# Kernel tuning notes

Measured on AMD Instinct MI355X. Metric: run time of the kernel, lower is better.

Reference implementation:

```python
import jax, jax.numpy as jnp
import numpy as np
import math

B, S, D, H = 8, 1024, 1024, 16
DK = D          # d_k = d_v = d_model (required for the per-head matmul to type-check)
HD = DK // H    # per-head dim = 64


def setup_inputs() -> dict:
    key = jax.random.key(0)
    ks = jax.random.split(key, 10)
    sc = 0.02
    return {
        "source": jax.random.normal(ks[0], (B, S, D), dtype=jnp.float32),
        "target": jax.random.normal(ks[1], (B, S, D), dtype=jnp.float32),
        "wq": jax.random.normal(ks[2], (D, DK), dtype=jnp.float32) * sc,
        "wk": jax.random.normal(ks[3], (D, DK), dtype=jnp.float32) * sc,
        "wv": jax.random.normal(ks[4], (D, DK), dtype=jnp.float32) * sc,
        "WQ": jax.random.normal(ks[5], (H, D, HD), dtype=jnp.float32) * sc,
        "WK": jax.random.normal(ks[6], (H, D, HD), dtype=jnp.float32) * sc,
        "WV": jax.random.normal(ks[7], (H, D, HD), dtype=jnp.float32) * sc,
        "ow": jax.random.normal(ks[8], (DK, D), dtype=jnp.float32) * sc,
        "ob": jnp.zeros((D,), dtype=jnp.float32),
    }


def reference(source, target, wq, wk, wv, WQ, WK, WV, ow, ob):
    # shared projections (nn.Linear, bias=False)
    Q = source @ wq          # (B,S,DK)
    K = target @ wk          # (B,S,DK)
    V = target @ wv          # (B,S,DK)
    # per-head projections Q @ W_Q[i], vectorized over all heads
    q = jnp.einsum('bsk,hkd->bhsd', Q, WQ)   # (B,H,S,HD)
    k = jnp.einsum('bsk,hkd->bhsd', K, WK)
    v = jnp.einsum('bsk,hkd->bhsd', V, WV)
    scores = jnp.einsum('bhqd,bhkd->bhqk', q, k) / math.sqrt(DK)
    # NOTE: original uses nn.Softmax(dim=1) on (B, Sq, Sk) -> normalizes over
    # the QUERY axis; faithful translation => axis=2 of (B,H,Sq,Sk).
    attn = jax.nn.softmax(scores, axis=2)
    o = jnp.einsum('bhqk,bhkd->bhqd', attn, v)          # (B,H,S,HD)
    o = jnp.transpose(o, (0, 2, 1, 3)).reshape(B, S, DK)  # concat heads
    return o @ ow + ob
```

## Files before the change

kernel.cpp:

```cpp
#include <hip/hip_runtime.h>

using u16 = unsigned short;
typedef float f32x4 __attribute__((ext_vector_type(4)));
typedef __bf16 bf16x8 __attribute__((ext_vector_type(8)));
typedef unsigned short u16x4 __attribute__((ext_vector_type(4)));
typedef unsigned short u16x8 __attribute__((ext_vector_type(8)));
typedef unsigned int u32x2 __attribute__((ext_vector_type(2)));

static constexpr float SC2 = 0.03125f * 1.44269504088896f;

static __device__ __forceinline__ u16 f2bf(float f) {
  unsigned u = __builtin_bit_cast(unsigned, f);
  u += 0x7FFFu + ((u >> 16) & 1u);
  return (u16)(u >> 16);
}
static __device__ __forceinline__ float bf2f(u16 h) {
  unsigned u = ((unsigned)h) << 16;
  return __builtin_bit_cast(float, u);
}
static __device__ __forceinline__ unsigned cvt_pk(float lo, float hi) {
  unsigned r;
  asm("v_cvt_pk_bf16_f32 %0, %1, %2" : "=v"(r) : "v"(lo), "v"(hi));
  return r;
}

typedef __attribute__((address_space(3))) unsigned int lds_uint;
typedef __attribute__((address_space(1))) unsigned int g_uint;

static __device__ __forceinline__ void load_lds16(const u16* gp, const void* lp) {
  __builtin_amdgcn_global_load_lds((g_uint*)(unsigned long long)gp,
                                   (lds_uint*)(unsigned int)(unsigned long long)lp,
                                   16, 0, 0);
}

struct Cast2 { const float* in[2]; u16* out[2]; };
__global__ __launch_bounds__(256) void k_cast2(Cast2 P, int n4) {
  int i = blockIdx.x * 256 + threadIdx.x;
  if (i >= n4) return;
  f32x4 v = reinterpret_cast<const f32x4*>(P.in[blockIdx.z])[i];
  u16x4 o;
  o[0] = f2bf(v[0]); o[1] = f2bf(v[1]); o[2] = f2bf(v[2]); o[3] = f2bf(v[3]);
  reinterpret_cast<u16x4*>(P.out[blockIdx.z])[i] = o;
}
struct Cast3 { const float* in[3]; u16* out[3]; };
__global__ __launch_bounds__(256) void k_cast3(Cast3 P, int n4) {
  int i = blockIdx.x * 256 + threadIdx.x;
  if (i >= n4) return;
  f32x4 v = reinterpret_cast<const f32x4*>(P.in[blockIdx.z])[i];
  u16x4 o;
  o[0] = f2bf(v[0]); o[1] = f2bf(v[1]); o[2] = f2bf(v[2]); o[3] = f2bf(v[3]);
  reinterpret_cast<u16x4*>(P.out[blockIdx.z])[i] = o;
}

__global__ __launch_bounds__(256) void k_relayout_W3(Cast3 P) {
  int idx = blockIdx.x * 256 + threadIdx.x;
  int n = idx >> 10, c = idx & 1023;
  int h = n >> 6, j = n & 63;
  P.out[blockIdx.z][idx] = f2bf(P.in[blockIdx.z][(h * 1024 + c) * 64 + j]);
}

__global__ __launch_bounds__(256) void k_relayout_owT(const float* __restrict__ ow,
                                                      u16* __restrict__ out) {
  int idx = blockIdx.x * 256 + threadIdx.x;
  int n = idx >> 10, k = idx & 1023;
  out[idx] = f2bf(ow[k * 1024 + n]);
}

struct GemmPtrs { const u16* A; const u16* B; void* C; float scale; };
struct Gemm3 { GemmPtrs g[3]; };

__global__ __launch_bounds__(256) void k_gemm_bt(Gemm3 P, int N, int K,
                                                 const float* __restrict__ bias,
                                                 int outf32) {
  const u16* A  = P.g[blockIdx.z].A;
  const u16* Bt = P.g[blockIdx.z].B;
  const float sc = P.g[blockIdx.z].scale;
  __shared__ u16 As[2][128 * 64];
  __shared__ u16 Bs[2][128 * 64];
  const int tid = threadIdx.x, lane = tid & 63, w = tid >> 6;
  const int swz = (blockIdx.x & 7) * (gridDim.x >> 3) + (blockIdx.x >> 3);
  const int nbn = N >> 7;
  const int m0 = (swz / nbn) << 7;
  const int n0 = (swz % nbn) << 7;
  const int wr = (w >> 1) << 6, wc = (w & 1) << 6;
  const int l15 = lane & 15, lg = lane >> 4;
  const int srow = tid >> 3;
  const int sslot = (tid & 7) ^ (srow & 7);
  const u16* Ag = A  + (size_t)(m0 + srow) * K + sslot * 8;
  const u16* Bg = Bt + (size_t)(n0 + srow) * K + sslot * 8;

  f32x4 acc[4][4];
#pragma unroll
  for (int i = 0; i < 4; ++i)
#pragma unroll
    for (int j = 0; j < 4; ++j) acc[i][j] = f32x4{0.f, 0.f, 0.f, 0.f};

#pragma unroll
  for (int j = 0; j < 4; ++j) {
    load_lds16(Ag + (size_t)(j * 32) * K, (const char*)As[0] + j * 4096 + tid * 16);
    load_lds16(Bg + (size_t)(j * 32) * K, (const char*)Bs[0] + j * 4096 + tid * 16);
  }
  __syncthreads();

  for (int kt = 0; kt < K; kt += 64) {
    const int buf = (kt >> 6) & 1;
    if (kt + 64 < K) {
#pragma unroll
      for (int j = 0; j < 4; ++j) {
        load_lds16(Ag + (size_t)(j * 32) * K + kt + 64, (const char*)As[buf ^ 1] + j * 4096 + tid * 16);
        load_lds16(Bg + (size_t)(j * 32) * K + kt + 64, (const char*)Bs[buf ^ 1] + j * 4096 + tid * 16);
      }
    }
#pragma unroll
    for (int kh = 0; kh < 2; ++kh) {
      bf16x8 af[4], bfr[4];
#pragma unroll
      for (int i = 0; i < 4; ++i) {
        const int ra = wr + i * 16 + l15;
        const int rb = wc + i * 16 + l15;
        af[i]  = *reinterpret_cast<const bf16x8*>(As[buf] + ra * 64 + ((((kh << 2) | lg) ^ (ra & 7)) << 3));
        bfr[i] = *reinterpret_cast<const bf16x8*>(Bs[buf] + rb * 64 + ((((kh << 2) | lg) ^ (rb & 7)) << 3));
      }
#pragma unroll
      for (int mi = 0; mi < 4; ++mi)
#pragma unroll
        for (int ni = 0; ni < 4; ++ni)
          acc[mi][ni] = __builtin_amdgcn_mfma_f32_16x16x32_bf16(af[mi], bfr[ni], acc[mi][ni], 0, 0, 0);
    }
    __syncthreads();
  }

  const int orow0 = m0 + wr + lg * 4;
  const int ocol0 = n0 + wc + l15;
  if (outf32) {
    float* C = (float*)P.g[blockIdx.z].C;
#pragma unroll
    for (int ni = 0; ni < 4; ++ni) {
      float bv = bias ? bias[ocol0 + ni * 16] : 0.f;
#pragma unroll
      for (int mi = 0; mi < 4; ++mi)
#pragma unroll
        for (int r = 0; r < 4; ++r)
          C[(size_t)(orow0 + mi * 16 + r) * N + ocol0 + ni * 16] = acc[mi][ni][r] + bv;
    }
  } else {
    u16* C = (u16*)P.g[blockIdx.z].C;
#pragma unroll
    for (int ni = 0; ni < 4; ++ni)
#pragma unroll
      for (int mi = 0; mi < 4; ++mi)
#pragma unroll
        for (int r = 0; r < 4; ++r)
          C[(size_t)(orow0 + mi * 16 + r) * N + ocol0 + ni * 16] = f2bf(acc[mi][ni][r] * sc);
  }
}

__global__ __launch_bounds__(256) void k_pass1(const u16* __restrict__ q_all,
                                               const u16* __restrict__ k_all,
                                               float* __restrict__ l_buf) {
  const int bh = blockIdx.x, kb = blockIdx.y;
  const int b = bh >> 4, h = bh & 15;
  __shared__ u16 Qs[2][2048];
  const int t = threadIdx.x;
  const int lane = t & 63, w = t >> 6;
  const int l15 = lane & 15, lg = lane >> 4;
  const u16* qp = q_all + (size_t)b * 1048576 + h * 64;
  const u16* kp = k_all + (size_t)b * 1048576 + h * 64;
  const int kc0 = kb * 128 + w * 32;

  bf16x8 bfr[2][2];
#pragma unroll
  for (int c = 0; c < 2; ++c)
#pragma unroll
    for (int ks = 0; ks < 2; ++ks)
      bfr[c][ks] = *reinterpret_cast<const bf16x8*>(
          kp + (size_t)(kc0 + c * 16 + l15) * 1024 + ks * 32 + lg * 8);

  const int qrow = t >> 3, qslot = (t & 7) ^ (qrow & 7);
  const u16* qg = qp + (size_t)qrow * 1024 + (qslot << 3);

  load_lds16(qg, (const char*)&Qs[0][0] + t * 16);
  __syncthreads();

  float acc0 = 0.f, acc1 = 0.f;
  const int qsw = l15 & 7;

#pragma unroll 1
  for (int qt = 0; qt < 1024; qt += 32) {
    const int buf = (qt >> 5) & 1;
    if (qt + 32 < 1024)
      load_lds16(qg + (size_t)(qt + 32) * 1024, (const char*)&Qs[buf ^ 1][0] + t * 16);
    const u16* Qb = Qs[buf];
    bf16x8 aq[2][2];
#pragma unroll
    for (int qf = 0; qf < 2; ++qf) {
      aq[qf][0] = *reinterpret_cast<const bf16x8*>(Qb + (qf * 16 + l15) * 64 + ((lg ^ qsw) << 3));
      aq[qf][1] = *reinterpret_cast<const bf16x8*>(Qb + (qf * 16 + l15) * 64 + (((4 + lg) ^ qsw) << 3));
    }
#pragma unroll
    for (int qf = 0; qf < 2; ++qf)
#pragma unroll
      for (int c = 0; c < 2; ++c) {
        f32x4 z = {0.f, 0.f, 0.f, 0.f};
        f32x4 s = __builtin_amdgcn_mfma_f32_16x16x32_bf16(aq[qf][0], bfr[c][0], z, 0, 0, 0);
        s = __builtin_amdgcn_mfma_f32_16x16x32_bf16(aq[qf][1], bfr[c][1], s, 0, 0, 0);
        float e = __builtin_amdgcn_exp2f(s[0]) + __builtin_amdgcn_exp2f(s[1])
                + __builtin_amdgcn_exp2f(s[2]) + __builtin_amdgcn_exp2f(s[3]);
        if (c) acc1 += e; else acc0 += e;
      }
    __syncthreads();
  }
  acc0 += __shfl_xor(acc0, 16); acc0 += __shfl_xor(acc0, 32);
  acc1 += __shfl_xor(acc1, 16); acc1 += __shfl_xor(acc1, 32);
  if (lane < 32) {
    int col = kc0 + lane;
    l_buf[(size_t)bh * 1024 + col] = (lane < 16) ? acc0 : acc1;
  }
}

__global__ __launch_bounds__(256) void k_transpose_v(const u16* __restrict__ v_all,
                                                     const float* __restrict__ l_buf,
                                                     u16* __restrict__ vT) {
  const int bh = blockIdx.x, kb = blockIdx.y;
  const int b = bh >> 4, h = bh & 15;
  __shared__ float tile[64][65];
  const int t = threadIdx.x;
#pragma unroll
  for (int i = 0; i < 2; ++i) {
    int idx = i * 256 + t;
    int kk = idx >> 3, ch = (idx & 7) * 8;
    float rl = 1.0f / l_buf[(size_t)bh * 1024 + kb * 64 + kk];
    u16x8 vv = *reinterpret_cast<const u16x8*>(
        v_all + ((size_t)(b * 1024 + kb * 64 + kk)) * 1024 + h * 64 + ch);
#pragma unroll
    for (int j = 0; j < 8; ++j) tile[kk][ch + j] = bf2f(vv[j]) * rl;
  }
  __syncthreads();
#pragma unroll
  for (int i = 0; i < 2; ++i) {
    int idx = i * 256 + t;
    int d = idx >> 3, kc = (idx & 7) * 8;
    u16x8 pv;
#pragma unroll
    for (int j = 0; j < 8; ++j) pv[j] = f2bf(tile[kc + j][d]);
    *reinterpret_cast<u16x8*>(vT + ((size_t)bh * 64 + d) * 1024 + kb * 64 + kc) = pv;
  }
}

__global__ __launch_bounds__(256, 4) void k_pass2(const u16* __restrict__ q_all,
                                                  const u16* __restrict__ k_all,
                                                  const u16* __restrict__ vT,
                                                  u16* __restrict__ o_all) {
  const int bh = blockIdx.x, qb = blockIdx.y;
  const int b = bh >> 4, h = bh & 15;
  __shared__ u16 Ks[2][2048];
  __shared__ u16 Vs[2][2048];
  __shared__ u16 p_lds[4][2][2][640];
  const int t = threadIdx.x;
  const int lane = t & 63, w = t >> 6;
  const int l15 = lane & 15, lg = lane >> 4;
  const int q0 = qb * 128 + w * 32;
  const u16* qp = q_all + (size_t)b * 1048576 + h * 64;
  const u16* kp = k_all + (size_t)b * 1048576 + h * 64;
  const u16* vp = vT + (size_t)bh * 65536;

  const int krow = t >> 3, kslot = (t & 7) ^ (krow & 7);
  const u16* kg = kp + (size_t)krow * 1024 + (kslot << 3);
  const int vrow = t >> 2, vslot = (t & 3) ^ (vrow & 3);
  const u16* vg = vp + (size_t)vrow * 1024 + (vslot << 3);

  bf16x8 bq[2][2];
#pragma unroll
  for (int qf = 0; qf < 2; ++qf)
#pragma unroll
    for (int s = 0; s < 2; ++s)
      bq[qf][s] = *reinterpret_cast<const bf16x8*>(
          qp + (size_t)(q0 + qf * 16 + l15) * 1024 + s * 32 + lg * 8);

  f32x4 od[2][4];
#pragma unroll
  for (int qf = 0; qf < 2; ++qf)
#pragma unroll
    for (int n = 0; n < 4; ++n) od[qf][n] = f32x4{0.f, 0.f, 0.f, 0.f};

  load_lds16(kg, (const char*)&Ks[0][0] + t * 16);
  load_lds16(vg, (const char*)&Vs[0][0] + t * 16);
  __syncthreads();

  const int ksw = l15 & 7, vsw = l15 & 3;

#pragma unroll 1
  for (int kt = 0; kt < 1024; kt += 32) {
    const int buf = (kt >> 5) & 1;
    if (kt + 32 < 1024) {
      load_lds16(kg + (size_t)(kt + 32) * 1024, (const char*)&Ks[buf ^ 1][0] + t * 16);
      load_lds16(vg + (kt + 32), (const char*)&Vs[buf ^ 1][0] + t * 16);
    }
    const u16* Kb = Ks[buf];
    const u16* Vb = Vs[buf];
    bf16x8 k00 = *reinterpret_cast<const bf16x8*>(Kb + l15 * 64 + ((lg ^ ksw) << 3));
    bf16x8 k01 = *reinterpret_cast<const bf16x8*>(Kb + l15 * 64 + (((4 + lg) ^ ksw) << 3));
    bf16x8 k10 = *reinterpret_cast<const bf16x8*>(Kb + (16 + l15) * 64 + ((lg ^ ksw) << 3));
    bf16x8 k11 = *reinterpret_cast<const bf16x8*>(Kb + (16 + l15) * 64 + (((4 + lg) ^ ksw) << 3));
    bf16x8 vc[4];
#pragma unroll
    for (int n = 0; n < 4; ++n)
      vc[n] = *reinterpret_cast<const bf16x8*>(Vb + (n * 16 + l15) * 32 + ((lg ^ vsw) << 3));

    u16* pl = p_lds[w][buf][0];
    u16* ph = p_lds[w][buf][1];
#pragma unroll
    for (int qf = 0; qf < 2; ++qf) {
      f32x4 z = {0.f, 0.f, 0.f, 0.f};
      f32x4 s0 = __builtin_amdgcn_mfma_f32_16x16x32_bf16(k00, bq[qf][0], z, 0, 0, 0);
      s0 = __builtin_amdgcn_mfma_f32_16x16x32_bf16(k01, bq[qf][1], s0, 0, 0, 0);
      f32x4 s1 = __builtin_amdgcn_mfma_f32_16x16x32_bf16(k10, bq[qf][0], z, 0, 0, 0);
      s1 = __builtin_amdgcn_mfma_f32_16x16x32_bf16(k11, bq[qf][1], s1, 0, 0, 0);
      u32x2 wlo, whi;
      wlo[0] = cvt_pk(__builtin_amdgcn_exp2f(s0[0]), __builtin_amdgcn_exp2f(s0[1]));
      wlo[1] = cvt_pk(__builtin_amdgcn_exp2f(s0[2]), __builtin_amdgcn_exp2f(s0[3]));
      whi[0] = cvt_pk(__builtin_amdgcn_exp2f(s1[0]), __builtin_amdgcn_exp2f(s1[1]));
      whi[1] = cvt_pk(__builtin_amdgcn_exp2f(s1[2]), __builtin_amdgcn_exp2f(s1[3]));
      u16* dst = qf ? ph : pl;
      *reinterpret_cast<u32x2*>(dst + l15 * 40 + lg * 4) = wlo;
      *reinterpret_cast<u32x2*>(dst + l15 * 40 + 16 + lg * 4) = whi;
    }
    bf16x8 pa0 = *reinterpret_cast<const bf16x8*>(pl + l15 * 40 + lg * 8);
    bf16x8 pa1 = *reinterpret_cast<const bf16x8*>(ph + l15 * 40 + lg * 8);
#pragma unroll
    for (int n = 0; n < 4; ++n) {
      od[0][n] = __builtin_amdgcn_mfma_f32_16x16x32_bf16(pa0, vc[n], od[0][n], 0, 0, 0);
      od[1][n] = __builtin_amdgcn_mfma_f32_16x16x32_bf16(pa1, vc[n], od[1][n], 0, 0, 0);
    }
    __syncthreads();
  }

  u16* op = o_all + (size_t)b * 1048576 + h * 64;
#pragma unroll
  for (int qf = 0; qf < 2; ++qf)
#pragma unroll
    for (int n = 0; n < 4; ++n)
#pragma unroll
      for (int r = 0; r < 4; ++r)
        op[(size_t)(q0 + qf * 16 + lg * 4 + r) * 1024 + n * 16 + l15] = f2bf(od[qf][n][r]);
}

extern "C" void kernel_launch(void* const* d_in, const int* in_sizes, int n_in,
                              void* d_out, int out_size, void* d_ws, size_t ws_size,
                              hipStream_t stream) {
  (void)in_sizes; (void)n_in; (void)out_size; (void)ws_size;
  char* base = (char*)d_ws;
  size_t off = 0;
  auto alloc = [&](size_t bytes) -> char* {
    char* p = base + off;
    off = (off + bytes + 255) & ~(size_t)255;
    return p;
  };
  u16* src_bf = (u16*)alloc(8ull * 1024 * 1024 * 2);
  u16* tgt_bf = (u16*)alloc(8ull * 1024 * 1024 * 2);
  u16* wq_bf  = (u16*)alloc(1024 * 1024 * 2);
  u16* wk_bf  = (u16*)alloc(1024 * 1024 * 2);
  u16* wv_bf  = (u16*)alloc(1024 * 1024 * 2);
  u16* WQt    = (u16*)alloc(1024 * 1024 * 2);
  u16* WKt    = (u16*)alloc(1024 * 1024 * 2);
  u16* WVt    = (u16*)alloc(1024 * 1024 * 2);
  u16* CqT    = (u16*)alloc(1024 * 1024 * 2);
  u16* CkT    = (u16*)alloc(1024 * 1024 * 2);
  u16* CvT    = (u16*)alloc(1024 * 1024 * 2);
  u16* owT    = (u16*)alloc(1024 * 1024 * 2);
  u16* q_all  = (u16*)alloc(8ull * 1024 * 1024 * 2);
  u16* k_all  = (u16*)alloc(8ull * 1024 * 1024 * 2);
  u16* v_all  = (u16*)alloc(8ull * 1024 * 1024 * 2);
  u16* vT     = (u16*)alloc(8ull * 1024 * 1024 * 2);
  u16* o_all  = (u16*)alloc(8ull * 1024 * 1024 * 2);
  float* l_buf = (float*)alloc(128 * 1024 * 4);

  Cast2 c2 = {{(const float*)d_in[0], (const float*)d_in[1]}, {src_bf, tgt_bf}};
  k_cast2<<<dim3(8192, 1, 2), 256, 0, stream>>>(c2, 2097152);
  Cast3 c3 = {{(const float*)d_in[2], (const float*)d_in[3], (const float*)d_in[4]},
              {wq_bf, wk_bf, wv_bf}};
  k_cast3<<<dim3(1024, 1, 3), 256, 0, stream>>>(c3, 262144);
  Cast3 w3 = {{(const float*)d_in[5], (const float*)d_in[6], (const float*)d_in[7]},
              {WQt, WKt, WVt}};
  k_relayout_W3<<<dim3(4096, 1, 3), 256, 0, stream>>>(w3);
  k_relayout_owT<<<4096, 256, 0, stream>>>((const float*)d_in[8], owT);

  Gemm3 comb = {{{WQt, wq_bf, CqT, SC2}, {WKt, wk_bf, CkT, 1.f}, {WVt, wv_bf, CvT, 1.f}}};
  k_gemm_bt<<<dim3(64, 1, 3), 256, 0, stream>>>(comb, 1024, 1024, nullptr, 0);

  Gemm3 proj = {{{src_bf, CqT, q_all, 1.f}, {tgt_bf, CkT, k_all, 1.f}, {tgt_bf, CvT, v_all, 1.f}}};
  k_gemm_bt<<<dim3(512, 1, 3), 256, 0, stream>>>(proj, 1024, 1024, nullptr, 0);

  k_pass1<<<dim3(128, 8), 256, 0, stream>>>(q_all, k_all, l_buf);
  k_transpose_v<<<dim3(128, 16), 256, 0, stream>>>(v_all, l_buf, vT);
  k_pass2<<<dim3(128, 8), 256, 0, stream>>>(q_all, k_all, vT, o_all);

  Gemm3 fin = {{{o_all, owT, d_out, 1.f}, {o_all, owT, d_out, 1.f}, {o_all, owT, d_out, 1.f}}};
  k_gemm_bt<<<dim3(512, 1, 1), 256, 0, stream>>>(fin, 1024, 1024, (const float*)d_in[9], 1);
}
```

Baseline: 225.2 us.

## Fuse V transpose into projection GEMM epilogue and apply 1/l in pass2

The V projection GEMM now writes its output directly in the transposed per-head layout that pass2 consumes, which removes the separate transpose kernel and the intermediate v_all buffer. The per-key softmax normalization (1/l) moves from the transpose step into pass2: reciprocals are staged in shared memory and multiplied into the exponentials before the bf16 pack. The cost is strided 8-byte stores in the GEMM epilogue instead of row-coalesced writes, plus extra multiplies and shared-memory reads inside pass2's inner loop.

```diff
diff --git a/kernel.cpp b/kernel.cpp
--- a/kernel.cpp
+++ b/kernel.cpp
@@ -66,15 +66,15 @@
   out[idx] = f2bf(ow[k * 1024 + n]);
 }
 
-struct GemmPtrs { const u16* A; const u16* B; void* C; float scale; };
+struct GemmPtrs { const u16* A; const u16* B; void* C; float scale; int mode; };
 struct Gemm3 { GemmPtrs g[3]; };
 
 __global__ __launch_bounds__(256) void k_gemm_bt(Gemm3 P, int N, int K,
-                                                 const float* __restrict__ bias,
-                                                 int outf32) {
+                                                 const float* __restrict__ bias) {
   const u16* A  = P.g[blockIdx.z].A;
   const u16* Bt = P.g[blockIdx.z].B;
   const float sc = P.g[blockIdx.z].scale;
+  const int mode = P.g[blockIdx.z].mode;
   __shared__ u16 As[2][128 * 64];
   __shared__ u16 Bs[2][128 * 64];
   const int tid = threadIdx.x, lane = tid & 63, w = tid >> 6;
@@ -132,7 +132,7 @@
 
   const int orow0 = m0 + wr + lg * 4;
   const int ocol0 = n0 + wc + l15;
-  if (outf32) {
+  if (mode == 1) {
     float* C = (float*)P.g[blockIdx.z].C;
 #pragma unroll
     for (int ni = 0; ni < 4; ++ni) {
@@ -142,6 +142,23 @@
 #pragma unroll
         for (int r = 0; r < 4; ++r)
           C[(size_t)(orow0 + mi * 16 + r) * N + ocol0 + ni * 16] = acc[mi][ni][r] + bv;
+    }
+  } else if (mode == 2) {
+    u16* C = (u16*)P.g[blockIdx.z].C;
+    const int b = m0 >> 10;
+    const int kk0 = (orow0 & 1023);
+#pragma unroll
+    for (int ni = 0; ni < 4; ++ni) {
+      const int col = ocol0 + ni * 16;
+      const int hh = col >> 6, d = col & 63;
+      u16* vbase = C + ((size_t)(b * 16 + hh)) * 65536 + d * 1024 + kk0;
+#pragma unroll
+      for (int mi = 0; mi < 4; ++mi) {
+        u16x4 pv;
+#pragma unroll
+        for (int r = 0; r < 4; ++r) pv[r] = f2bf(acc[mi][ni][r] * sc);
+        *reinterpret_cast<u16x4*>(vbase + mi * 16) = pv;
+      }
     }
   } else {
     u16* C = (u16*)P.g[blockIdx.z].C;
@@ -218,44 +235,17 @@
   }
 }
 
-__global__ __launch_bounds__(256) void k_transpose_v(const u16* __restrict__ v_all,
-                                                     const float* __restrict__ l_buf,
-                                                     u16* __restrict__ vT) {
-  const int bh = blockIdx.x, kb = blockIdx.y;
-  const int b = bh >> 4, h = bh & 15;
-  __shared__ float tile[64][65];
-  const int t = threadIdx.x;
-#pragma unroll
-  for (int i = 0; i < 2; ++i) {
-    int idx = i * 256 + t;
-    int kk = idx >> 3, ch = (idx & 7) * 8;
-    float rl = 1.0f / l_buf[(size_t)bh * 1024 + kb * 64 + kk];
-    u16x8 vv = *reinterpret_cast<const u16x8*>(
-        v_all + ((size_t)(b * 1024 + kb * 64 + kk)) * 1024 + h * 64 + ch);
-#pragma unroll
-    for (int j = 0; j < 8; ++j) tile[kk][ch + j] = bf2f(vv[j]) * rl;
-  }
-  __syncthreads();
-#pragma unroll
-  for (int i = 0; i < 2; ++i) {
-    int idx = i * 256 + t;
-    int d = idx >> 3, kc = (idx & 7) * 8;
-    u16x8 pv;
-#pragma unroll
-    for (int j = 0; j < 8; ++j) pv[j] = f2bf(tile[kc + j][d]);
-    *reinterpret_cast<u16x8*>(vT + ((size_t)bh * 64 + d) * 1024 + kb * 64 + kc) = pv;
-  }
-}
-
 __global__ __launch_bounds__(256, 4) void k_pass2(const u16* __restrict__ q_all,
                                                   const u16* __restrict__ k_all,
                                                   const u16* __restrict__ vT,
+                                                  const float* __restrict__ l_buf,
                                                   u16* __restrict__ o_all) {
   const int bh = blockIdx.x, qb = blockIdx.y;
   const int b = bh >> 4, h = bh & 15;
   __shared__ u16 Ks[2][2048];
   __shared__ u16 Vs[2][2048];
   __shared__ u16 p_lds[4][2][2][640];
+  __shared__ float rl_lds[1024];
   const int t = threadIdx.x;
   const int lane = t & 63, w = t >> 6;
   const int l15 = lane & 15, lg = lane >> 4;
@@ -264,6 +254,14 @@
   const u16* kp = k_all + (size_t)b * 1048576 + h * 64;
   const u16* vp = vT + (size_t)bh * 65536;
 
+  {
+    f32x4 lv = reinterpret_cast<const f32x4*>(l_buf + (size_t)bh * 1024)[t];
+    f32x4 rv;
+#pragma unroll
+    for (int j = 0; j < 4; ++j) rv[j] = 1.0f / lv[j];
+    reinterpret_cast<f32x4*>(rl_lds)[t] = rv;
+  }
+
   const int krow = t >> 3, kslot = (t & 7) ^ (krow & 7);
   const u16* kg = kp + (size_t)krow * 1024 + (kslot << 3);
   const int vrow = t >> 2, vslot = (t & 3) ^ (vrow & 3);
@@ -307,6 +305,9 @@
     for (int n = 0; n < 4; ++n)
       vc[n] = *reinterpret_cast<const bf16x8*>(Vb + (n * 16 + l15) * 32 + ((lg ^ vsw) << 3));
 
+    f32x4 r0 = *reinterpret_cast<const f32x4*>(&rl_lds[kt + lg * 4]);
+    f32x4 r1 = *reinterpret_cast<const f32x4*>(&rl_lds[kt + 16 + lg * 4]);
+
     u16* pl = p_lds[w][buf][0];
     u16* ph = p_lds[w][buf][1];
 #pragma unroll
@@ -317,10 +318,10 @@
       f32x4 s1 = __builtin_amdgcn_mfma_f32_16x16x32_bf16(k10, bq[qf][0], z, 0, 0, 0);
       s1 = __builtin_amdgcn_mfma_f32_16x16x32_bf16(k11, bq[qf][1], s1, 0, 0, 0);
       u32x2 wlo, whi;
-      wlo[0] = cvt_pk(__builtin_amdgcn_exp2f(s0[0]), __builtin_amdgcn_exp2f(s0[1]));
-      wlo[1] = cvt_pk(__builtin_amdgcn_exp2f(s0[2]), __builtin_amdgcn_exp2f(s0[3]));
-      whi[0] = cvt_pk(__builtin_amdgcn_exp2f(s1[0]), __builtin_amdgcn_exp2f(s1[1]));
-      whi[1] = cvt_pk(__builtin_amdgcn_exp2f(s1[2]), __builtin_amdgcn_exp2f(s1[3]));
+      wlo[0] = cvt_pk(__builtin_amdgcn_exp2f(s0[0]) * r0[0], __builtin_amdgcn_exp2f(s0[1]) * r0[1]);
+      wlo[1] = cvt_pk(__builtin_amdgcn_exp2f(s0[2]) * r0[2], __builtin_amdgcn_exp2f(s0[3]) * r0[3]);
+      whi[0] = cvt_pk(__builtin_amdgcn_exp2f(s1[0]) * r1[0], __builtin_amdgcn_exp2f(s1[1]) * r1[1]);
+      whi[1] = cvt_pk(__builtin_amdgcn_exp2f(s1[2]) * r1[2], __builtin_amdgcn_exp2f(s1[3]) * r1[3]);
       u16* dst = qf ? ph : pl;
       *reinterpret_cast<u32x2*>(dst + l15 * 40 + lg * 4) = wlo;
       *reinterpret_cast<u32x2*>(dst + l15 * 40 + 16 + lg * 4) = whi;
@@ -370,7 +371,6 @@
   u16* owT    = (u16*)alloc(1024 * 1024 * 2);
   u16* q_all  = (u16*)alloc(8ull * 1024 * 1024 * 2);
   u16* k_all  = (u16*)alloc(8ull * 1024 * 1024 * 2);
-  u16* v_all  = (u16*)alloc(8ull * 1024 * 1024 * 2);
   u16* vT     = (u16*)alloc(8ull * 1024 * 1024 * 2);
   u16* o_all  = (u16*)alloc(8ull * 1024 * 1024 * 2);
   float* l_buf = (float*)alloc(128 * 1024 * 4);
@@ -385,16 +385,15 @@
   k_relayout_W3<<<dim3(4096, 1, 3), 256, 0, stream>>>(w3);
   k_relayout_owT<<<4096, 256, 0, stream>>>((const float*)d_in[8], owT);
 
-  Gemm3 comb = {{{WQt, wq_bf, CqT, SC2}, {WKt, wk_bf, CkT, 1.f}, {WVt, wv_bf, CvT, 1.f}}};
-  k_gemm_bt<<<dim3(64, 1, 3), 256, 0, stream>>>(comb, 1024, 1024, nullptr, 0);
-
-  Gemm3 proj = {{{src_bf, CqT, q_all, 1.f}, {tgt_bf, CkT, k_all, 1.f}, {tgt_bf, CvT, v_all, 1.f}}};
-  k_gemm_bt<<<dim3(512, 1, 3), 256, 0, stream>>>(proj, 1024, 1024, nullptr, 0);
+  Gemm3 comb = {{{WQt, wq_bf, CqT, SC2, 0}, {WKt, wk_bf, CkT, 1.f, 0}, {WVt, wv_bf, CvT, 1.f, 0}}};
+  k_gemm_bt<<<dim3(64, 1, 3), 256, 0, stream>>>(comb, 1024, 1024, nullptr);
+
+  Gemm3 proj = {{{src_bf, CqT, q_all, 1.f, 0}, {tgt_bf, CkT, k_all, 1.f, 0}, {tgt_bf, CvT, vT, 1.f, 2}}};
+  k_gemm_bt<<<dim3(512, 1, 3), 256, 0, stream>>>(proj, 1024, 1024, nullptr);
 
   k_pass1<<<dim3(128, 8), 256, 0, stream>>>(q_all, k_all, l_buf);
-  k_transpose_v<<<dim3(128, 16), 256, 0, stream>>>(v_all, l_buf, vT);
-  k_pass2<<<dim3(128, 8), 256, 0, stream>>>(q_all, k_all, vT, o_all);
-
-  Gemm3 fin = {{{o_all, owT, d_out, 1.f}, {o_all, owT, d_out, 1.f}, {o_all, owT, d_out, 1.f}}};
-  k_gemm_bt<<<dim3(512, 1, 1), 256, 0, stream>>>(fin, 1024, 1024, (const float*)d_in[9], 1);
-}
+  k_pass2<<<dim3(128, 8), 256, 0, stream>>>(q_all, k_all, vT, l_buf, o_all);
+
+  Gemm3 fin = {{{o_all, owT, d_out, 1.f, 1}, {o_all, owT, d_out, 1.f, 1}, {o_all, owT, d_out, 1.f, 1}}};
+  k_gemm_bt<<<dim3(512, 1, 1), 256, 0, stream>>>(fin, 1024, 1024, (const float*)d_in[9]);
+}
```

Measured after the change: 220.6 us. 1.02x faster.
